# Kernel optimization log

Hardware: AMD Instinct MI355X
Metric: run time of the kernel (lower is better)

Reference implementation:

```python
import jax, jax.numpy as jnp
import numpy as np

D0, D1, D2, D3 = 128, 256, 512, 256
B, L = 64, 1024


def _glorot(key, shape):
    fan_in = shape[0]
    return jax.random.normal(key, shape, dtype=jnp.float32) / np.sqrt(fan_in)


def setup_inputs() -> dict:
    key = jax.random.key(0)
    ks = jax.random.split(key, 16)
    return {
        "hid_r": jax.random.normal(ks[0], (B, L, D3), dtype=jnp.float32),
        "in_mask": jnp.ones((B, L), dtype=jnp.float32),
        "init_in": jnp.zeros((B, 1, D0), dtype=jnp.float32),
        "h0": jnp.zeros((1, B, D2), dtype=jnp.float32),
        "c0": jnp.zeros((1, B, D2), dtype=jnp.float32),
        # lin_1: D0 -> D1 (Linear + ReLU)
        "W1": _glorot(ks[1], (D0, D1)), "b1": jnp.zeros((D1,), jnp.float32),
        # LSTM: input D1, hidden D2, gates order i,f,g,o (PyTorch)
        "Wih": _glorot(ks[2], (D1, 4 * D2)), "Whh": _glorot(ks[3], (D2, 4 * D2)),
        "bih": jnp.zeros((4 * D2,), jnp.float32), "bhh": jnp.zeros((4 * D2,), jnp.float32),
        # lin_2: D2 -> D3
        "W2": _glorot(ks[4], (D2, D3)), "b2": jnp.zeros((D3,), jnp.float32),
        # attention projections q,k,v (D3 -> D3)
        "Wq": _glorot(ks[5], (D3, D3)), "bq": jnp.zeros((D3,), jnp.float32),
        "Wk": _glorot(ks[6], (D3, D3)), "bk": jnp.zeros((D3,), jnp.float32),
        "Wv": _glorot(ks[7], (D3, D3)), "bv": jnp.zeros((D3,), jnp.float32),
        # lin_3: D3 -> D0
        "W3": _glorot(ks[8], (D3, D0)), "b3": jnp.zeros((D0,), jnp.float32),
    }


def reference(hid_r, in_mask, init_in, h0, c0, W1, b1, Wih, Whh, bih, bhh,
              W2, b2, Wq, bq, Wk, bk, Wv, bv, W3, b3):
    length = hid_r.shape[1]
    scale = 1.0 / np.sqrt(D3).astype(np.float32)
    # k/v projections of the (fixed) encoder memory, hoisted out of the loop
    k = hid_r @ Wk + bk            # [B, L, D3]
    v = hid_r @ Wv + bv            # [B, L, D3]
    mask_bias = jnp.where(in_mask == 0, -1e9, 0.0)  # [B, L]

    def step(carry, _):
        h, c, x = carry            # h,c: [B,D2], x: [B,D0]
        a = jax.nn.relu(x @ W1 + b1)                       # lin_1
        gates = a @ Wih + bih + h @ Whh + bhh              # [B, 4*D2]
        i_g, f_g, g_g, o_g = jnp.split(gates, 4, axis=-1)
        c = jax.nn.sigmoid(f_g) * c + jax.nn.sigmoid(i_g) * jnp.tanh(g_g)
        h = jax.nn.sigmoid(o_g) * jnp.tanh(c)
        dx = jax.nn.relu(h @ W2 + b2)                      # lin_2 -> [B,D3]
        q = dx @ Wq + bq                                   # [B, D3]
        scores = jnp.einsum('bd,bld->bl', q, k) * scale + mask_bias
        attn = jax.nn.softmax(scores, axis=-1)             # [B, L]
        ctx = jnp.einsum('bl,bld->bd', attn, v)            # [B, D3]
        y = jax.nn.relu(ctx @ W3 + b3)                     # lin_3 -> [B,D0]
        return (h, c, y), (y, attn)

    carry0 = (h0[0], c0[0], init_in[:, 0, :])
    _, (ys, attns) = jax.lax.scan(step, carry0, None, length=length)
    outputs = jnp.transpose(ys, (1, 0, 2)) * in_mask[:, :, None]  # mask_it
    attention_weights = jnp.transpose(attns, (1, 0, 2))           # [B, L, L]
    return outputs, attention_weights
```

## Files before the change

kernel.cpp:

```cpp
#include <hip/hip_runtime.h>

typedef unsigned short u16;
typedef __attribute__((ext_vector_type(8))) short bf16x8;
typedef __attribute__((ext_vector_type(8))) unsigned short u16x8;
typedef __attribute__((ext_vector_type(4))) unsigned short u16x4;
typedef __attribute__((ext_vector_type(4))) float f32x4;

#define DI static __device__ __forceinline__

constexpr size_t OFF_WKQ  = 0;
constexpr size_t OFF_WVW  = OFF_WKQ  + 256*256*4;
constexpr size_t OFF_WB   = OFF_WVW  + 256*128*4;
constexpr size_t OFF_BYV  = OFF_WB   + 256*4;
constexpr size_t OFF_BG   = OFF_BYV  + 128*4;
constexpr size_t OFF_W2B  = OFF_BG   + 2048*4;
constexpr size_t OFF_W1F  = OFF_W2B  + 512*256*2;
constexpr size_t OFF_WIHF = OFF_W1F  + 16*4*64*8*2;
constexpr size_t OFF_WHHF = OFF_WIHF + 128*8*64*8*2;
constexpr size_t OFF_KT   = OFF_WHHF + 128*16*64*8*2;
constexpr size_t OFF_VW   = OFF_KT   + (size_t)64*1024*256*2;
constexpr size_t OFF_S0   = OFF_VW   + (size_t)64*1024*128*2;
constexpr size_t OFF_CB   = OFF_S0   + 65536*4;
constexpr size_t OFF_HF   = OFF_CB   + 64*512*4;
constexpr size_t OFF_HFR  = OFF_HF   + 64*512*4;
constexpr size_t OFF_SC   = OFF_HFR  + 2*16*4*64*8*2;
constexpr size_t OFF_PART = OFF_SC   + 64*1024*4;

DI float bf2f(u16 u){ unsigned int v = ((unsigned int)u) << 16; return __uint_as_float(v); }
DI u16 f2bf(float f){ unsigned int u = __float_as_uint(f); unsigned int r = (u + 0x7FFFu + ((u>>16)&1u)) >> 16; return (u16)r; }
DI float sigm(float x){ return 1.f/(1.f + __expf(-x)); }
DI float tanh_(float x){ return 1.f - 2.f/(__expf(2.f*x) + 1.f); }

DI int fragIdx(int m, int k){ return (((k>>5)*4 + (m>>4))*64 + ((m&15) | (((k>>3)&3)<<4)))*8 + (k&7); }

__global__ __launch_bounds__(256) void kPrep(char* ws,
    const float* W1, const float* Wih, const float* Whh, const float* W2,
    const float* Wq, const float* bq, const float* Wk, const float* bk,
    const float* Wv, const float* bv, const float* W3, const float* b3,
    const float* bih, const float* bhh, const float* c0, const float* h0)
{
  const int wg = blockIdx.x, tid = threadIdx.x;
  if (wg < 64) {
    float* Wkq = (float*)(ws + OFF_WKQ);
    for (int rr = 0; rr < 4; ++rr) {
      const int e = wg*4 + rr;
      float acc = 0.f;
      for (int d = 0; d < 256; ++d) acc = fmaf(Wk[e*256+d], Wq[tid*256+d], acc);
      Wkq[e*256 + tid] = acc * 0.0625f;
    }
  } else if (wg < 96) {
    float* Wvw = (float*)(ws + OFF_WVW);
    if (tid < 128) {
      for (int rr = 0; rr < 8; ++rr) {
        const int e = (wg-64)*8 + rr;
        float acc = 0.f;
        for (int d = 0; d < 256; ++d) acc = fmaf(Wv[e*256+d], W3[d*128+tid], acc);
        Wvw[e*128 + tid] = acc;
      }
    }
  } else if (wg == 96) {
    float* wb = (float*)(ws + OFF_WB);
    float acc = 0.f;
    for (int d = 0; d < 256; ++d) acc = fmaf(Wk[tid*256+d], bq[d], acc);
    wb[tid] = acc * 0.0625f;
    if (tid < 128) {
      float* byv = (float*)(ws + OFF_BYV);
      float a2 = b3[tid];
      for (int d = 0; d < 256; ++d) a2 = fmaf(bv[d], W3[d*128+tid], a2);
      byv[tid] = a2;
    }
  } else if (wg == 97) {
    float* bg = (float*)(ws + OFF_BG);
    for (int j = tid; j < 2048; j += 256) bg[j] = bih[j] + bhh[j];
  } else if (wg < 106) {
    u16* W2b = (u16*)(ws + OFF_W2B);
    const int r0 = (wg - 98)*64;
    for (int rr = 0; rr < 64; ++rr) W2b[(r0+rr)*256 + tid] = f2bf(W2[(r0+rr)*256 + tid]);
  } else if (wg < 122) {
    u16* W1f = (u16*)(ws + OFF_W1F);
    const int nt2 = wg - 106;
    for (int idx = tid; idx < 4*512; idx += 256) {
      const int kt2 = idx >> 9, rem = idx & 511, lane = rem >> 3, i = rem & 7;
      const int k = kt2*32 + (lane>>4)*8 + i, n = nt2*16 + (lane&15);
      W1f[((nt2*4+kt2)*64+lane)*8+i] = f2bf(W1[k*256+n]);
    }
  } else if (wg < 250) {
    u16* Wihf = (u16*)(ws + OFF_WIHF);
    const int nt = wg - 122;
    for (int idx = tid; idx < 8*512; idx += 256) {
      const int kt = idx >> 9, rem = idx & 511, lane = rem >> 3, i = rem & 7;
      const int k = kt*32 + (lane>>4)*8 + i, r = lane & 15;
      const int gcol = (r>>2)*512 + nt*4 + (r&3);
      Wihf[((nt*8+kt)*64+lane)*8+i] = f2bf(Wih[k*2048 + gcol]);
    }
  } else if (wg < 378) {
    u16* Whhf = (u16*)(ws + OFF_WHHF);
    const int nt = wg - 250;
    for (int idx = tid; idx < 16*512; idx += 256) {
      const int kt = idx >> 9, rem = idx & 511, lane = rem >> 3, i = rem & 7;
      const int k = kt*32 + (lane>>4)*8 + i, r = lane & 15;
      const int gcol = (r>>2)*512 + nt*4 + (r&3);
      Whhf[((nt*16+kt)*64+lane)*8+i] = f2bf(Whh[k*2048 + gcol]);
    }
  } else if (wg < 410) {
    float* cb = (float*)(ws + OFF_CB);
    u16* hfr0 = (u16*)(ws + OFF_HFR);
    const int base = (wg - 378)*1024;
    for (int ii = tid; ii < 1024; ii += 256) {
      const int idx = base + ii, b = idx >> 9, j = idx & 511;
      cb[idx] = c0[idx];
      hfr0[fragIdx(b, j)] = f2bf(h0[idx]);
    }
  }
}

__global__ __launch_bounds__(256) void kKTVW(char* __restrict__ ws, const float* __restrict__ hid_r)
{
  const int wg = blockIdx.x, tid = threadIdx.x;
  __shared__ float lh[256*36];
  const float* Wkq = (const float*)(ws + OFF_WKQ);
  const float* Wvw = (const float*)(ws + OFF_WVW);
  const float* wb  = (const float*)(ws + OFF_WB);
  u16* kt = (u16*)(ws + OFF_KT);
  u16* vw = (u16*)(ws + OFF_VW);
  float* s0 = (float*)(ws + OFF_S0);
  const size_t r0 = (size_t)wg * 32;
  for (int idx = tid; idx < 32*256; idx += 256) {
    const int e = idx & 255, r = idx >> 8;
    lh[e*36 + r] = hid_r[(r0 + r)*256 + e];
  }
  __syncthreads();
  float acc[32];
  #pragma unroll
  for (int r = 0; r < 32; ++r) acc[r] = 0.f;
  for (int e = 0; e < 256; ++e) {
    const float wv = Wkq[e*256 + tid];
    #pragma unroll
    for (int r4 = 0; r4 < 8; ++r4) {
      const float4 l4 = *(const float4*)&lh[e*36 + r4*4];
      acc[r4*4+0] = fmaf(l4.x, wv, acc[r4*4+0]);
      acc[r4*4+1] = fmaf(l4.y, wv, acc[r4*4+1]);
      acc[r4*4+2] = fmaf(l4.z, wv, acc[r4*4+2]);
      acc[r4*4+3] = fmaf(l4.w, wv, acc[r4*4+3]);
    }
  }
  for (int r = 0; r < 32; ++r) kt[(r0 + r)*256 + tid] = f2bf(acc[r]);
  if (tid < 128) {
    #pragma unroll
    for (int r = 0; r < 32; ++r) acc[r] = 0.f;
    for (int e = 0; e < 256; ++e) {
      const float wv = Wvw[e*128 + tid];
      #pragma unroll
      for (int r4 = 0; r4 < 8; ++r4) {
        const float4 l4 = *(const float4*)&lh[e*36 + r4*4];
        acc[r4*4+0] = fmaf(l4.x, wv, acc[r4*4+0]);
        acc[r4*4+1] = fmaf(l4.y, wv, acc[r4*4+1]);
        acc[r4*4+2] = fmaf(l4.z, wv, acc[r4*4+2]);
        acc[r4*4+3] = fmaf(l4.w, wv, acc[r4*4+3]);
      }
    }
    for (int r = 0; r < 32; ++r) vw[(r0 + r)*128 + tid] = f2bf(acc[r]);
  } else if (tid < 160) {
    const int r = tid - 128;
    float a3 = 0.f;
    for (int e = 0; e < 256; ++e) a3 = fmaf(lh[e*36 + r], wb[e], a3);
    s0[r0 + r] = a3;
  }
}

__global__ __launch_bounds__(512) void kA(char* __restrict__ ws, const float* __restrict__ init_in,
    const float* __restrict__ in_mask, const float* __restrict__ b1, float* __restrict__ dout, int s)
{
  const int wg = blockIdx.x, tid = threadIdx.x;
  float* part = (float*)(ws + OFF_PART);
  float* scores = (float*)(ws + OFF_SC);

  if (wg >= 128) {
    if (s == 0) return;
    const int b = (wg - 128) >> 1, half = (wg - 128) & 1;
    float pm[4], pS[4], m = -1e30f;
    #pragma unroll
    for (int c = 0; c < 4; ++c) { pm[c] = part[(b*4+c)*130]; pS[c] = part[(b*4+c)*130+1]; m = fmaxf(m, pm[c]); }
    float Sv = 0.f;
    #pragma unroll
    for (int c = 0; c < 4; ++c) Sv += pS[c] * __expf(pm[c]-m);
    const float inv = 1.f / Sv;
    const int t = s - 1;
    const int l = half*512 + tid;
    float* attn = dout + (size_t)64*1024*128;
    attn[((size_t)b*1024 + t)*1024 + l] = __expf(scores[b*1024 + l] - m) * inv;
    if (half == 0 && tid < 128) {
      const float* byv = (const float*)(ws + OFF_BYV);
      float a2 = 0.f;
      #pragma unroll
      for (int c = 0; c < 4; ++c) a2 += __expf(pm[c]-m) * part[(b*4+c)*130+2+tid];
      const float y = fmaxf(a2*inv + byv[tid], 0.f);
      dout[((size_t)b*1024 + t)*128 + tid] = y * in_mask[b*1024 + t];
    }
    return;
  }

  __shared__ u16 yfrag[4*4*64*8];
  __shared__ u16 afrag[8*4*64*8];
  __shared__ float lfac[64*4];
  __shared__ float gmerge[4*64*4];
  __shared__ float gtile[64*16];
  const float* byv = (const float*)(ws + OFF_BYV);

  if (s == 0) {
    for (int idx = tid; idx < 64*128; idx += 512) {
      const int b = idx >> 7, d0 = idx & 127;
      yfrag[fragIdx(b, d0)] = f2bf(init_in[b*128 + d0]);
    }
  } else {
    if (tid < 64) {
      const int b = tid;
      float pm[4], m = -1e30f;
      #pragma unroll
      for (int c = 0; c < 4; ++c) { pm[c] = part[(b*4+c)*130]; m = fmaxf(m, pm[c]); }
      float Sv = 0.f, pf[4];
      #pragma unroll
      for (int c = 0; c < 4; ++c) { pf[c] = __expf(pm[c]-m); Sv += part[(b*4+c)*130+1]*pf[c]; }
      const float inv = 1.f/Sv;
      #pragma unroll
      for (int c = 0; c < 4; ++c) lfac[b*4+c] = pf[c]*inv;
    }
    __syncthreads();
    for (int idx = tid; idx < 64*128; idx += 512) {
      const int b = idx >> 7, d0 = idx & 127;
      float a2 = byv[d0];
      #pragma unroll
      for (int c = 0; c < 4; ++c) a2 += lfac[b*4+c]*part[(b*4+c)*130+2+d0];
      yfrag[fragIdx(b, d0)] = f2bf(fmaxf(a2, 0.f));
    }
  }
  __syncthreads();

  const int w = tid >> 6, lane = tid & 63;
  {
    const u16* W1f = (const u16*)(ws + OFF_W1F);
    const int mt = w & 3;
    for (int nb = 0; nb < 8; ++nb) {
      const int nt2 = (w>>2)*8 + nb;
      f32x4 acc = {0.f,0.f,0.f,0.f};
      #pragma unroll
      for (int kt2 = 0; kt2 < 4; ++kt2) {
        bf16x8 av = *(const bf16x8*)&yfrag[((kt2*4+mt)*64+lane)*8];
        bf16x8 bv = *(const bf16x8*)&W1f[((nt2*4+kt2)*64+lane)*8];
        acc = __builtin_amdgcn_mfma_f32_16x16x32_bf16(av, bv, acc, 0, 0, 0);
      }
      const int col = nt2*16 + (lane&15);
      const float bb = b1[col];
      #pragma unroll
      for (int i = 0; i < 4; ++i) {
        const int b = mt*16 + (lane>>4)*4 + i;
        afrag[fragIdx(b, col)] = f2bf(fmaxf(acc[i] + bb, 0.f));
      }
    }
  }
  __syncthreads();
  {
    const u16* Wihf = (const u16*)(ws + OFF_WIHF);
    const u16* Whhf = (const u16*)(ws + OFF_WHHF);
    const u16* hfr = (const u16*)(ws + OFF_HFR) + (size_t)(s & 1)*(16*4*64*8);
    const int nt = wg, mt = w & 3;
    f32x4 acc = {0.f,0.f,0.f,0.f};
    if (w < 4) {
      for (int kt = 0; kt < 8; ++kt) {
        bf16x8 av = *(const bf16x8*)&afrag[((kt*4+mt)*64+lane)*8];
        bf16x8 bv = *(const bf16x8*)&Wihf[((nt*8+kt)*64+lane)*8];
        acc = __builtin_amdgcn_mfma_f32_16x16x32_bf16(av, bv, acc, 0, 0, 0);
      }
      for (int kt = 0; kt < 4; ++kt) {
        bf16x8 av = *(const bf16x8*)&hfr[((kt*4+mt)*64+lane)*8];
        bf16x8 bv = *(const bf16x8*)&Whhf[((nt*16+kt)*64+lane)*8];
        acc = __builtin_amdgcn_mfma_f32_16x16x32_bf16(av, bv, acc, 0, 0, 0);
      }
    } else {
      for (int kt = 4; kt < 16; ++kt) {
        bf16x8 av = *(const bf16x8*)&hfr[((kt*4+mt)*64+lane)*8];
        bf16x8 bv = *(const bf16x8*)&Whhf[((nt*16+kt)*64+lane)*8];
        acc = __builtin_amdgcn_mfma_f32_16x16x32_bf16(av, bv, acc, 0, 0, 0);
      }
      #pragma unroll
      for (int i = 0; i < 4; ++i) gmerge[(mt*64+lane)*4+i] = acc[i];
    }
    __syncthreads();
    if (w < 4) {
      const float* bg = (const float*)(ws + OFF_BG);
      const int r = lane & 15;
      const float bb = bg[(r>>2)*512 + nt*4 + (r&3)];
      #pragma unroll
      for (int i = 0; i < 4; ++i) {
        const int b = mt*16 + (lane>>4)*4 + i;
        gtile[b*16 + r] = acc[i] + gmerge[(mt*64+lane)*4+i] + bb;
      }
    }
  }
  __syncthreads();
  if (tid < 256) {
    const int b = tid >> 2, jj = tid & 3;
    const int j = wg*4 + jj;
    const float ig = gtile[b*16 + jj],     fg = gtile[b*16 + 4 + jj];
    const float gg = gtile[b*16 + 8 + jj], og = gtile[b*16 + 12 + jj];
    float* cb = (float*)(ws + OFF_CB);
    float* hf = (float*)(ws + OFF_HF);
    u16* hfw = (u16*)(ws + OFF_HFR) + (size_t)((s & 1) ^ 1)*(16*4*64*8);
    const float cold = cb[b*512 + j];
    const float cnew = sigm(fg)*cold + sigm(ig)*tanh_(gg);
    const float hnew = sigm(og)*tanh_(cnew);
    cb[b*512 + j] = cnew;
    hf[b*512 + j] = hnew;
    hfw[fragIdx(b, j)] = f2bf(hnew);
  }
}

__global__ __launch_bounds__(1024) void kB(char* __restrict__ ws, const float* __restrict__ in_mask,
                                           const float* __restrict__ b2, int s)
{
  const int wg = blockIdx.x, tid = threadIdx.x;
  const int b = wg >> 2, ch = wg & 3;
  __shared__ float red[4*256];
  __shared__ float dxl[256];
  __shared__ float mrg[32*132];
  const float* hf = (const float*)(ws + OFF_HF);
  const u16* W2b = (const u16*)(ws + OFF_W2B);
  (void)s;
  {
    const int n = tid & 255, q = tid >> 8;
    const float* hb = hf + b*512;
    float acc = 0.f;
    #pragma unroll 4
    for (int k = q*128; k < q*128 + 128; ++k)
      acc = fmaf(hb[k], bf2f(W2b[k*256 + n]), acc);
    red[q*256 + n] = acc;
  }
  __syncthreads();
  if (tid < 256) dxl[tid] = fmaxf(red[tid] + red[256+tid] + red[512+tid] + red[768+tid] + b2[tid], 0.f);
  __syncthreads();

  const int hl = tid & 31;
  const int unit = tid >> 5;
  float dxv[8];
  #pragma unroll
  for (int j2 = 0; j2 < 8; ++j2) dxv[j2] = dxl[hl*8 + j2];
  const u16* kt = (const u16*)(ws + OFF_KT);
  const u16* vw = (const u16*)(ws + OFF_VW);
  const float* s0 = (const float*)(ws + OFF_S0);
  float m = -1e30f, S = 0.f, cx0 = 0.f, cx1 = 0.f, cx2 = 0.f, cx3 = 0.f, keep = 0.f;
  for (int i = 0; i < 8; ++i) {
    const int l = ch*256 + i*32 + unit;
    const size_t row = (size_t)b*1024 + l;
    const u16x8 kv = *(const u16x8*)(kt + row*256 + hl*8);
    float sum = 0.f;
    #pragma unroll
    for (int j2 = 0; j2 < 8; ++j2) sum = fmaf(bf2f(kv[j2]), dxv[j2], sum);
    #pragma unroll
    for (int d = 1; d < 32; d <<= 1) sum += __shfl_xor(sum, d, 64);
    float sc = sum + s0[row];
    sc += (in_mask[row] == 0.f) ? -1e9f : 0.f;
    if (hl == i) keep = sc;
    const float mn = fmaxf(m, sc);
    const float cf = __expf(m - mn);
    const float e  = __expf(sc - mn);
    S = S*cf + e;
    cx0 *= cf; cx1 *= cf; cx2 *= cf; cx3 *= cf;
    m = mn;
    const u16x4 vv = *(const u16x4*)(vw + row*128 + hl*4);
    cx0 = fmaf(e, bf2f(vv[0]), cx0);
    cx1 = fmaf(e, bf2f(vv[1]), cx1);
    cx2 = fmaf(e, bf2f(vv[2]), cx2);
    cx3 = fmaf(e, bf2f(vv[3]), cx3);
  }
  if (hl < 8) ((float*)(ws + OFF_SC))[b*1024 + ch*256 + hl*32 + unit] = keep;
  mrg[unit*132 + 4 + hl*4 + 0] = cx0;
  mrg[unit*132 + 4 + hl*4 + 1] = cx1;
  mrg[unit*132 + 4 + hl*4 + 2] = cx2;
  mrg[unit*132 + 4 + hl*4 + 3] = cx3;
  if (hl == 0) { mrg[unit*132] = m; mrg[unit*132+1] = S; }
  __syncthreads();
  if (tid < 128) {
    float mg = -1e30f;
    for (int u = 0; u < 32; ++u) mg = fmaxf(mg, mrg[u*132]);
    float Sg = 0.f, cx = 0.f;
    for (int u = 0; u < 32; ++u) {
      const float f = __expf(mrg[u*132] - mg);
      Sg = fmaf(mrg[u*132+1], f, Sg);
      cx = fmaf(f, mrg[u*132 + 4 + tid], cx);
    }
    float* part = (float*)(ws + OFF_PART);
    part[(b*4+ch)*130 + 2 + tid] = cx;
    if (tid == 0) { part[(b*4+ch)*130] = mg; part[(b*4+ch)*130+1] = Sg; }
  }
}

extern "C" void kernel_launch(void* const* d_in, const int* in_sizes, int n_in,
                              void* d_out, int out_size, void* d_ws, size_t ws_size,
                              hipStream_t stream)
{
  (void)in_sizes; (void)n_in; (void)out_size; (void)ws_size;
  const float* hid_r  = (const float*)d_in[0];
  const float* in_mask= (const float*)d_in[1];
  const float* init_in= (const float*)d_in[2];
  const float* h0     = (const float*)d_in[3];
  const float* c0     = (const float*)d_in[4];
  const float* W1     = (const float*)d_in[5];
  const float* b1     = (const float*)d_in[6];
  const float* Wih    = (const float*)d_in[7];
  const float* Whh    = (const float*)d_in[8];
  const float* bih    = (const float*)d_in[9];
  const float* bhh    = (const float*)d_in[10];
  const float* W2     = (const float*)d_in[11];
  const float* b2     = (const float*)d_in[12];
  const float* Wq     = (const float*)d_in[13];
  const float* bq     = (const float*)d_in[14];
  const float* Wk     = (const float*)d_in[15];
  const float* bk     = (const float*)d_in[16];
  const float* Wv     = (const float*)d_in[17];
  const float* bv     = (const float*)d_in[18];
  const float* W3     = (const float*)d_in[19];
  const float* b3     = (const float*)d_in[20];
  char* ws = (char*)d_ws;
  float* out = (float*)d_out;

  hipLaunchKernelGGL(kPrep, dim3(410), dim3(256), 0, stream, ws,
                     W1, Wih, Whh, W2, Wq, bq, Wk, bk, Wv, bv, W3, b3, bih, bhh, c0, h0);
  hipLaunchKernelGGL(kKTVW, dim3(2048), dim3(256), 0, stream, ws, hid_r);
  for (int s = 0; s < 1024; ++s) {
    hipLaunchKernelGGL(kA, dim3(256), dim3(512), 0, stream, ws, init_in, in_mask, b1, out, s);
    hipLaunchKernelGGL(kB, dim3(256), dim3(1024), 0, stream, ws, in_mask, b2, s);
  }
  hipLaunchKernelGGL(kA, dim3(256), dim3(512), 0, stream, ws, init_in, in_mask, b1, out, 1024);
}
```

Measured before the change: 32.48 ms.

## Fuse the recurrent loop into one persistent per-batch kernel with fp16 dot products

```diff
diff --git a/kernel.cpp b/kernel.cpp
--- a/kernel.cpp
+++ b/kernel.cpp
@@ -1,43 +1,44 @@
 #include <hip/hip_runtime.h>
 
 typedef unsigned short u16;
-typedef __attribute__((ext_vector_type(8))) short bf16x8;
-typedef __attribute__((ext_vector_type(8))) unsigned short u16x8;
-typedef __attribute__((ext_vector_type(4))) unsigned short u16x4;
-typedef __attribute__((ext_vector_type(4))) float f32x4;
+typedef unsigned int u32;
+typedef __attribute__((ext_vector_type(4))) unsigned int u32x4;
+typedef _Float16 half_t;
+typedef __attribute__((ext_vector_type(2))) _Float16 h2;
 
 #define DI static __device__ __forceinline__
 
-constexpr size_t OFF_WKQ  = 0;
-constexpr size_t OFF_WVW  = OFF_WKQ  + 256*256*4;
-constexpr size_t OFF_WB   = OFF_WVW  + 256*128*4;
-constexpr size_t OFF_BYV  = OFF_WB   + 256*4;
-constexpr size_t OFF_BG   = OFF_BYV  + 128*4;
-constexpr size_t OFF_W2B  = OFF_BG   + 2048*4;
-constexpr size_t OFF_W1F  = OFF_W2B  + 512*256*2;
-constexpr size_t OFF_WIHF = OFF_W1F  + 16*4*64*8*2;
-constexpr size_t OFF_WHHF = OFF_WIHF + 128*8*64*8*2;
-constexpr size_t OFF_KT   = OFF_WHHF + 128*16*64*8*2;
-constexpr size_t OFF_VW   = OFF_KT   + (size_t)64*1024*256*2;
-constexpr size_t OFF_S0   = OFF_VW   + (size_t)64*1024*128*2;
-constexpr size_t OFF_CB   = OFF_S0   + 65536*4;
-constexpr size_t OFF_HF   = OFF_CB   + 64*512*4;
-constexpr size_t OFF_HFR  = OFF_HF   + 64*512*4;
-constexpr size_t OFF_SC   = OFF_HFR  + 2*16*4*64*8*2;
-constexpr size_t OFF_PART = OFF_SC   + 64*1024*4;
-
-DI float bf2f(u16 u){ unsigned int v = ((unsigned int)u) << 16; return __uint_as_float(v); }
-DI u16 f2bf(float f){ unsigned int u = __float_as_uint(f); unsigned int r = (u + 0x7FFFu + ((u>>16)&1u)) >> 16; return (u16)r; }
+constexpr size_t OFF_WKQ = 0;
+constexpr size_t OFF_WVW = OFF_WKQ + 256*256*4;
+constexpr size_t OFF_WB  = OFF_WVW + 256*128*4;
+constexpr size_t OFF_BYV = OFF_WB  + 256*4;
+constexpr size_t OFF_BG  = OFF_BYV + 128*4;
+constexpr size_t OFF_W1H = OFF_BG  + 2048*4;
+constexpr size_t OFF_WGH = OFF_W1H + 128*256*2;
+constexpr size_t OFF_W2H = OFF_WGH + 768*2048*2;
+constexpr size_t OFF_S0  = OFF_W2H + 256*512*2;
+constexpr size_t OFF_KT2 = OFF_S0  + 65536*4;
+constexpr size_t OFF_VW2 = OFF_KT2 + (size_t)64*1024*256*2;
+
 DI float sigm(float x){ return 1.f/(1.f + __expf(-x)); }
 DI float tanh_(float x){ return 1.f - 2.f/(__expf(2.f*x) + 1.f); }
-
-DI int fragIdx(int m, int k){ return (((k>>5)*4 + (m>>4))*64 + ((m&15) | (((k>>3)&3)<<4)))*8 + (k&7); }
+DI u16 f2h(float f){ half_t h = (half_t)f; return __builtin_bit_cast(u16, h); }
+DI u32 pk2(float a, float b){ return (u32)f2h(a) | ((u32)f2h(b) << 16); }
+DI h2 u32h2(u32 v){ return __builtin_bit_cast(h2, v); }
+
+DI float fdot2f(h2 a, h2 b, float c){
+#if defined(__has_builtin) && __has_builtin(__builtin_amdgcn_fdot2)
+  return __builtin_amdgcn_fdot2(a, b, c, false);
+#else
+  return c + (float)a[0]*(float)b[0] + (float)a[1]*(float)b[1];
+#endif
+}
 
 __global__ __launch_bounds__(256) void kPrep(char* ws,
     const float* W1, const float* Wih, const float* Whh, const float* W2,
     const float* Wq, const float* bq, const float* Wk, const float* bk,
     const float* Wv, const float* bv, const float* W3, const float* b3,
-    const float* bih, const float* bhh, const float* c0, const float* h0)
+    const float* bih, const float* bhh)
 {
   const int wg = blockIdx.x, tid = threadIdx.x;
   if (wg < 64) {
@@ -73,56 +74,42 @@
     float* bg = (float*)(ws + OFF_BG);
     for (int j = tid; j < 2048; j += 256) bg[j] = bih[j] + bhh[j];
   } else if (wg < 106) {
-    u16* W2b = (u16*)(ws + OFF_W2B);
-    const int r0 = (wg - 98)*64;
-    for (int rr = 0; rr < 64; ++rr) W2b[(r0+rr)*256 + tid] = f2bf(W2[(r0+rr)*256 + tid]);
-  } else if (wg < 122) {
-    u16* W1f = (u16*)(ws + OFF_W1F);
-    const int nt2 = wg - 106;
-    for (int idx = tid; idx < 4*512; idx += 256) {
-      const int kt2 = idx >> 9, rem = idx & 511, lane = rem >> 3, i = rem & 7;
-      const int k = kt2*32 + (lane>>4)*8 + i, n = nt2*16 + (lane&15);
-      W1f[((nt2*4+kt2)*64+lane)*8+i] = f2bf(W1[k*256+n]);
-    }
-  } else if (wg < 250) {
-    u16* Wihf = (u16*)(ws + OFF_WIHF);
-    const int nt = wg - 122;
-    for (int idx = tid; idx < 8*512; idx += 256) {
-      const int kt = idx >> 9, rem = idx & 511, lane = rem >> 3, i = rem & 7;
-      const int k = kt*32 + (lane>>4)*8 + i, r = lane & 15;
-      const int gcol = (r>>2)*512 + nt*4 + (r&3);
-      Wihf[((nt*8+kt)*64+lane)*8+i] = f2bf(Wih[k*2048 + gcol]);
-    }
-  } else if (wg < 378) {
-    u16* Whhf = (u16*)(ws + OFF_WHHF);
-    const int nt = wg - 250;
-    for (int idx = tid; idx < 16*512; idx += 256) {
-      const int kt = idx >> 9, rem = idx & 511, lane = rem >> 3, i = rem & 7;
-      const int k = kt*32 + (lane>>4)*8 + i, r = lane & 15;
-      const int gcol = (r>>2)*512 + nt*4 + (r&3);
-      Whhf[((nt*16+kt)*64+lane)*8+i] = f2bf(Whh[k*2048 + gcol]);
-    }
-  } else if (wg < 410) {
-    float* cb = (float*)(ws + OFF_CB);
-    u16* hfr0 = (u16*)(ws + OFF_HFR);
-    const int base = (wg - 378)*1024;
-    for (int ii = tid; ii < 1024; ii += 256) {
-      const int idx = base + ii, b = idx >> 9, j = idx & 511;
-      cb[idx] = c0[idx];
-      hfr0[fragIdx(b, j)] = f2bf(h0[idx]);
-    }
-  }
-}
-
-__global__ __launch_bounds__(256) void kKTVW(char* __restrict__ ws, const float* __restrict__ hid_r)
+    u16* W1h = (u16*)(ws + OFF_W1H);
+    const int k0 = (wg - 98)*16;
+    for (int kk = 0; kk < 16; ++kk) {
+      const int k = k0 + kk;
+      W1h[((k>>3)*256 + tid)*8 + (k&7)] = f2h(W1[k*256 + tid]);
+    }
+  } else if (wg < 170) {
+    u16* Wgh = (u16*)(ws + OFF_WGH);
+    const int k0 = (wg - 106)*12;
+    for (int kk = 0; kk < 12; ++kk) {
+      const int k = k0 + kk;
+      for (int n = tid; n < 2048; n += 256) {
+        const float src = (k < 256) ? Wih[k*2048 + n] : Whh[(k-256)*2048 + n];
+        Wgh[((k>>3)*2048 + n)*8 + (k&7)] = f2h(src);
+      }
+    }
+  } else if (wg < 178) {
+    u16* W2h = (u16*)(ws + OFF_W2H);
+    const int n0 = (wg - 170)*32;
+    for (int nn = 0; nn < 32; ++nn) {
+      const int n = n0 + nn;
+      for (int k = tid; k < 512; k += 256) W2h[n*512 + k] = f2h(W2[k*256 + n]);
+    }
+  }
+}
+
+__global__ __launch_bounds__(256) void kKTVW(char* __restrict__ ws, const float* __restrict__ hid_r,
+                                             const float* __restrict__ in_mask)
 {
   const int wg = blockIdx.x, tid = threadIdx.x;
   __shared__ float lh[256*36];
   const float* Wkq = (const float*)(ws + OFF_WKQ);
   const float* Wvw = (const float*)(ws + OFF_WVW);
   const float* wb  = (const float*)(ws + OFF_WB);
-  u16* kt = (u16*)(ws + OFF_KT);
-  u16* vw = (u16*)(ws + OFF_VW);
+  u16* kt2 = (u16*)(ws + OFF_KT2);
+  u16* vw2 = (u16*)(ws + OFF_VW2);
   float* s0 = (float*)(ws + OFF_S0);
   const size_t r0 = (size_t)wg * 32;
   for (int idx = tid; idx < 32*256; idx += 256) {
@@ -144,7 +131,12 @@
       acc[r4*4+3] = fmaf(l4.w, wv, acc[r4*4+3]);
     }
   }
-  for (int r = 0; r < 32; ++r) kt[(r0 + r)*256 + tid] = f2bf(acc[r]);
+  for (int r = 0; r < 32; ++r) {
+    const size_t row = r0 + r;
+    const size_t bb = row >> 10;
+    const int l = (int)(row & 1023);
+    kt2[(((bb*32) + (size_t)(tid>>3))*1024 + l)*8 + (tid&7)] = f2h(acc[r]);
+  }
   if (tid < 128) {
     #pragma unroll
     for (int r = 0; r < 32; ++r) acc[r] = 0.f;
@@ -159,238 +151,206 @@
         acc[r4*4+3] = fmaf(l4.w, wv, acc[r4*4+3]);
       }
     }
-    for (int r = 0; r < 32; ++r) vw[(r0 + r)*128 + tid] = f2bf(acc[r]);
+    for (int r = 0; r < 32; ++r) {
+      const size_t row = r0 + r;
+      const size_t bb = row >> 10;
+      const int l = (int)(row & 1023);
+      vw2[((bb*512) + (size_t)(l>>1))*256 + tid*2 + (l&1)] = f2h(acc[r]);
+    }
   } else if (tid < 160) {
     const int r = tid - 128;
     float a3 = 0.f;
     for (int e = 0; e < 256; ++e) a3 = fmaf(lh[e*36 + r], wb[e], a3);
-    s0[r0 + r] = a3;
-  }
-}
-
-__global__ __launch_bounds__(512) void kA(char* __restrict__ ws, const float* __restrict__ init_in,
-    const float* __restrict__ in_mask, const float* __restrict__ b1, float* __restrict__ dout, int s)
+    s0[r0 + r] = a3 + (in_mask[r0 + r] == 0.f ? -1e9f : 0.f);
+  }
+}
+
+__global__ __launch_bounds__(1024) void kMain(char* __restrict__ ws, const float* __restrict__ init_in,
+    const float* __restrict__ in_mask, const float* __restrict__ b1g, const float* __restrict__ b2g,
+    const float* __restrict__ h0, const float* __restrict__ c0, float* __restrict__ dout)
 {
-  const int wg = blockIdx.x, tid = threadIdx.x;
-  float* part = (float*)(ws + OFF_PART);
-  float* scores = (float*)(ws + OFF_SC);
-
-  if (wg >= 128) {
-    if (s == 0) return;
-    const int b = (wg - 128) >> 1, half = (wg - 128) & 1;
-    float pm[4], pS[4], m = -1e30f;
-    #pragma unroll
-    for (int c = 0; c < 4; ++c) { pm[c] = part[(b*4+c)*130]; pS[c] = part[(b*4+c)*130+1]; m = fmaxf(m, pm[c]); }
-    float Sv = 0.f;
-    #pragma unroll
-    for (int c = 0; c < 4; ++c) Sv += pS[c] * __expf(pm[c]-m);
-    const float inv = 1.f / Sv;
-    const int t = s - 1;
-    const int l = half*512 + tid;
-    float* attn = dout + (size_t)64*1024*128;
-    attn[((size_t)b*1024 + t)*1024 + l] = __expf(scores[b*1024 + l] - m) * inv;
-    if (half == 0 && tid < 128) {
-      const float* byv = (const float*)(ws + OFF_BYV);
-      float a2 = 0.f;
-      #pragma unroll
-      for (int c = 0; c < 4; ++c) a2 += __expf(pm[c]-m) * part[(b*4+c)*130+2+tid];
-      const float y = fmaxf(a2*inv + byv[tid], 0.f);
-      dout[((size_t)b*1024 + t)*128 + tid] = y * in_mask[b*1024 + t];
-    }
-    return;
-  }
-
-  __shared__ u16 yfrag[4*4*64*8];
-  __shared__ u16 afrag[8*4*64*8];
-  __shared__ float lfac[64*4];
-  __shared__ float gmerge[4*64*4];
-  __shared__ float gtile[64*16];
+  const int b = blockIdx.x, tid = threadIdx.x;
+  const int hl = tid & 31, unit = tid >> 5;
+
+  __shared__ __align__(16) u32 x2[384];
+  __shared__ __align__(16) u32 yh2[64];
+  __shared__ __align__(16) u32 dxh2[128];
+  __shared__ __align__(16) u32 eh2[512];
+  __shared__ float gt[2048];
+  __shared__ float cst[512];
+  __shared__ float s0l[1024];
+  __shared__ float sc[1024];
+  __shared__ float red[256*33];
+  __shared__ float mrg[32*132];
+  __shared__ float rtmp[64];
+  __shared__ float fin[2];
+
+  const u16* W1h = (const u16*)(ws + OFF_W1H);
+  const u16* Wgh = (const u16*)(ws + OFF_WGH);
+  const u16* W2h = (const u16*)(ws + OFF_W2H);
+  const u16* kt2 = (const u16*)(ws + OFF_KT2) + (size_t)b*32*1024*8;
+  const u16* vw2 = (const u16*)(ws + OFF_VW2) + (size_t)b*512*256;
+  const float* s0g = (const float*)(ws + OFF_S0) + b*1024;
+  const float* bgg = (const float*)(ws + OFF_BG);
   const float* byv = (const float*)(ws + OFF_BYV);
-
-  if (s == 0) {
-    for (int idx = tid; idx < 64*128; idx += 512) {
-      const int b = idx >> 7, d0 = idx & 127;
-      yfrag[fragIdx(b, d0)] = f2bf(init_in[b*128 + d0]);
-    }
-  } else {
+  float* attn = dout + (size_t)64*1024*128;
+
+  if (tid < 512) cst[tid] = c0[b*512 + tid];
+  if (tid < 256) x2[128 + tid] = pk2(h0[b*512 + 2*tid], h0[b*512 + 2*tid + 1]);
+  if (tid < 64)  yh2[tid] = pk2(init_in[b*128 + 2*tid], init_in[b*128 + 2*tid + 1]);
+  s0l[tid] = s0g[tid];
+  __syncthreads();
+
+  for (int s = 0; s < 1024; ++s) {
+    if (tid < 256) {
+      float acc = b1g[tid];
+      #pragma unroll 4
+      for (int r = 0; r < 16; ++r) {
+        const u32x4 wv = *(const u32x4*)(W1h + ((r*256 + tid) << 3));
+        const u32x4 xq = *(const u32x4*)&yh2[r*4];
+        acc = fdot2f(u32h2(wv[0]), u32h2(xq[0]), acc);
+        acc = fdot2f(u32h2(wv[1]), u32h2(xq[1]), acc);
+        acc = fdot2f(u32h2(wv[2]), u32h2(xq[2]), acc);
+        acc = fdot2f(u32h2(wv[3]), u32h2(xq[3]), acc);
+      }
+      ((u16*)x2)[tid] = f2h(fmaxf(acc, 0.f));
+    }
+    __syncthreads();
+    {
+      float g0 = bgg[tid], g1 = bgg[tid + 1024];
+      #pragma unroll 4
+      for (int r = 0; r < 96; ++r) {
+        const u32x4 w0 = *(const u32x4*)(Wgh + (((r << 11) + tid) << 3));
+        const u32x4 w1 = *(const u32x4*)(Wgh + (((r << 11) + tid + 1024) << 3));
+        const u32x4 xq = *(const u32x4*)&x2[r*4];
+        g0 = fdot2f(u32h2(w0[0]), u32h2(xq[0]), g0);
+        g0 = fdot2f(u32h2(w0[1]), u32h2(xq[1]), g0);
+        g0 = fdot2f(u32h2(w0[2]), u32h2(xq[2]), g0);
+        g0 = fdot2f(u32h2(w0[3]), u32h2(xq[3]), g0);
+        g1 = fdot2f(u32h2(w1[0]), u32h2(xq[0]), g1);
+        g1 = fdot2f(u32h2(w1[1]), u32h2(xq[1]), g1);
+        g1 = fdot2f(u32h2(w1[2]), u32h2(xq[2]), g1);
+        g1 = fdot2f(u32h2(w1[3]), u32h2(xq[3]), g1);
+      }
+      gt[tid] = g0; gt[tid + 1024] = g1;
+    }
+    __syncthreads();
+    if (tid < 512) {
+      const float gi = gt[tid], gf = gt[512 + tid], gg = gt[1024 + tid], go = gt[1536 + tid];
+      const float cn = sigm(gf)*cst[tid] + sigm(gi)*tanh_(gg);
+      const float h  = sigm(go)*tanh_(cn);
+      cst[tid] = cn;
+      ((u16*)x2)[256 + tid] = f2h(h);
+    }
+    __syncthreads();
+    {
+      const u32x4 ha = *(const u32x4*)&x2[128 + hl*8];
+      const u32x4 hb = *(const u32x4*)&x2[128 + hl*8 + 4];
+      #pragma unroll
+      for (int j = 0; j < 8; ++j) {
+        const int n = unit*8 + j;
+        const u32x4 w0 = *(const u32x4*)(W2h + n*512 + hl*16);
+        const u32x4 w1 = *(const u32x4*)(W2h + n*512 + hl*16 + 8);
+        float acc = 0.f;
+        acc = fdot2f(u32h2(ha[0]), u32h2(w0[0]), acc);
+        acc = fdot2f(u32h2(ha[1]), u32h2(w0[1]), acc);
+        acc = fdot2f(u32h2(ha[2]), u32h2(w0[2]), acc);
+        acc = fdot2f(u32h2(ha[3]), u32h2(w0[3]), acc);
+        acc = fdot2f(u32h2(hb[0]), u32h2(w1[0]), acc);
+        acc = fdot2f(u32h2(hb[1]), u32h2(w1[1]), acc);
+        acc = fdot2f(u32h2(hb[2]), u32h2(w1[2]), acc);
+        acc = fdot2f(u32h2(hb[3]), u32h2(w1[3]), acc);
+        red[n*33 + hl] = acc;
+      }
+    }
+    __syncthreads();
+    if (tid < 256) {
+      float a = 0.f;
+      #pragma unroll
+      for (int l = 0; l < 32; ++l) a += red[tid*33 + l];
+      const float dx = fmaxf(a + b2g[tid], 0.f);
+      ((u16*)dxh2)[tid] = f2h(dx);
+    }
+    __syncthreads();
+    {
+      float st = s0l[tid];
+      #pragma unroll 4
+      for (int r = 0; r < 32; ++r) {
+        const u32x4 kv = __builtin_nontemporal_load((const u32x4*)(kt2 + (((size_t)r << 10) + tid)*8));
+        const u32x4 xq = *(const u32x4*)&dxh2[r*4];
+        st = fdot2f(u32h2(kv[0]), u32h2(xq[0]), st);
+        st = fdot2f(u32h2(kv[1]), u32h2(xq[1]), st);
+        st = fdot2f(u32h2(kv[2]), u32h2(xq[2]), st);
+        st = fdot2f(u32h2(kv[3]), u32h2(xq[3]), st);
+      }
+      sc[tid] = st;
+    }
+    __syncthreads();
     if (tid < 64) {
-      const int b = tid;
-      float pm[4], m = -1e30f;
-      #pragma unroll
-      for (int c = 0; c < 4; ++c) { pm[c] = part[(b*4+c)*130]; m = fmaxf(m, pm[c]); }
-      float Sv = 0.f, pf[4];
-      #pragma unroll
-      for (int c = 0; c < 4; ++c) { pf[c] = __expf(pm[c]-m); Sv += part[(b*4+c)*130+1]*pf[c]; }
-      const float inv = 1.f/Sv;
-      #pragma unroll
-      for (int c = 0; c < 4; ++c) lfac[b*4+c] = pf[c]*inv;
-    }
-    __syncthreads();
-    for (int idx = tid; idx < 64*128; idx += 512) {
-      const int b = idx >> 7, d0 = idx & 127;
-      float a2 = byv[d0];
-      #pragma unroll
-      for (int c = 0; c < 4; ++c) a2 += lfac[b*4+c]*part[(b*4+c)*130+2+d0];
-      yfrag[fragIdx(b, d0)] = f2bf(fmaxf(a2, 0.f));
-    }
-  }
-  __syncthreads();
-
-  const int w = tid >> 6, lane = tid & 63;
-  {
-    const u16* W1f = (const u16*)(ws + OFF_W1F);
-    const int mt = w & 3;
-    for (int nb = 0; nb < 8; ++nb) {
-      const int nt2 = (w>>2)*8 + nb;
-      f32x4 acc = {0.f,0.f,0.f,0.f};
-      #pragma unroll
-      for (int kt2 = 0; kt2 < 4; ++kt2) {
-        bf16x8 av = *(const bf16x8*)&yfrag[((kt2*4+mt)*64+lane)*8];
-        bf16x8 bv = *(const bf16x8*)&W1f[((nt2*4+kt2)*64+lane)*8];
-        acc = __builtin_amdgcn_mfma_f32_16x16x32_bf16(av, bv, acc, 0, 0, 0);
-      }
-      const int col = nt2*16 + (lane&15);
-      const float bb = b1[col];
-      #pragma unroll
-      for (int i = 0; i < 4; ++i) {
-        const int b = mt*16 + (lane>>4)*4 + i;
-        afrag[fragIdx(b, col)] = f2bf(fmaxf(acc[i] + bb, 0.f));
-      }
-    }
-  }
-  __syncthreads();
-  {
-    const u16* Wihf = (const u16*)(ws + OFF_WIHF);
-    const u16* Whhf = (const u16*)(ws + OFF_WHHF);
-    const u16* hfr = (const u16*)(ws + OFF_HFR) + (size_t)(s & 1)*(16*4*64*8);
-    const int nt = wg, mt = w & 3;
-    f32x4 acc = {0.f,0.f,0.f,0.f};
-    if (w < 4) {
-      for (int kt = 0; kt < 8; ++kt) {
-        bf16x8 av = *(const bf16x8*)&afrag[((kt*4+mt)*64+lane)*8];
-        bf16x8 bv = *(const bf16x8*)&Wihf[((nt*8+kt)*64+lane)*8];
-        acc = __builtin_amdgcn_mfma_f32_16x16x32_bf16(av, bv, acc, 0, 0, 0);
-      }
-      for (int kt = 0; kt < 4; ++kt) {
-        bf16x8 av = *(const bf16x8*)&hfr[((kt*4+mt)*64+lane)*8];
-        bf16x8 bv = *(const bf16x8*)&Whhf[((nt*16+kt)*64+lane)*8];
-        acc = __builtin_amdgcn_mfma_f32_16x16x32_bf16(av, bv, acc, 0, 0, 0);
-      }
-    } else {
-      for (int kt = 4; kt < 16; ++kt) {
-        bf16x8 av = *(const bf16x8*)&hfr[((kt*4+mt)*64+lane)*8];
-        bf16x8 bv = *(const bf16x8*)&Whhf[((nt*16+kt)*64+lane)*8];
-        acc = __builtin_amdgcn_mfma_f32_16x16x32_bf16(av, bv, acc, 0, 0, 0);
-      }
-      #pragma unroll
-      for (int i = 0; i < 4; ++i) gmerge[(mt*64+lane)*4+i] = acc[i];
-    }
-    __syncthreads();
-    if (w < 4) {
-      const float* bg = (const float*)(ws + OFF_BG);
-      const int r = lane & 15;
-      const float bb = bg[(r>>2)*512 + nt*4 + (r&3)];
-      #pragma unroll
-      for (int i = 0; i < 4; ++i) {
-        const int b = mt*16 + (lane>>4)*4 + i;
-        gtile[b*16 + r] = acc[i] + gmerge[(mt*64+lane)*4+i] + bb;
-      }
-    }
-  }
-  __syncthreads();
-  if (tid < 256) {
-    const int b = tid >> 2, jj = tid & 3;
-    const int j = wg*4 + jj;
-    const float ig = gtile[b*16 + jj],     fg = gtile[b*16 + 4 + jj];
-    const float gg = gtile[b*16 + 8 + jj], og = gtile[b*16 + 12 + jj];
-    float* cb = (float*)(ws + OFF_CB);
-    float* hf = (float*)(ws + OFF_HF);
-    u16* hfw = (u16*)(ws + OFF_HFR) + (size_t)((s & 1) ^ 1)*(16*4*64*8);
-    const float cold = cb[b*512 + j];
-    const float cnew = sigm(fg)*cold + sigm(ig)*tanh_(gg);
-    const float hnew = sigm(og)*tanh_(cnew);
-    cb[b*512 + j] = cnew;
-    hf[b*512 + j] = hnew;
-    hfw[fragIdx(b, j)] = f2bf(hnew);
-  }
-}
-
-__global__ __launch_bounds__(1024) void kB(char* __restrict__ ws, const float* __restrict__ in_mask,
-                                           const float* __restrict__ b2, int s)
-{
-  const int wg = blockIdx.x, tid = threadIdx.x;
-  const int b = wg >> 2, ch = wg & 3;
-  __shared__ float red[4*256];
-  __shared__ float dxl[256];
-  __shared__ float mrg[32*132];
-  const float* hf = (const float*)(ws + OFF_HF);
-  const u16* W2b = (const u16*)(ws + OFF_W2B);
-  (void)s;
-  {
-    const int n = tid & 255, q = tid >> 8;
-    const float* hb = hf + b*512;
-    float acc = 0.f;
-    #pragma unroll 4
-    for (int k = q*128; k < q*128 + 128; ++k)
-      acc = fmaf(hb[k], bf2f(W2b[k*256 + n]), acc);
-    red[q*256 + n] = acc;
-  }
-  __syncthreads();
-  if (tid < 256) dxl[tid] = fmaxf(red[tid] + red[256+tid] + red[512+tid] + red[768+tid] + b2[tid], 0.f);
-  __syncthreads();
-
-  const int hl = tid & 31;
-  const int unit = tid >> 5;
-  float dxv[8];
-  #pragma unroll
-  for (int j2 = 0; j2 < 8; ++j2) dxv[j2] = dxl[hl*8 + j2];
-  const u16* kt = (const u16*)(ws + OFF_KT);
-  const u16* vw = (const u16*)(ws + OFF_VW);
-  const float* s0 = (const float*)(ws + OFF_S0);
-  float m = -1e30f, S = 0.f, cx0 = 0.f, cx1 = 0.f, cx2 = 0.f, cx3 = 0.f, keep = 0.f;
-  for (int i = 0; i < 8; ++i) {
-    const int l = ch*256 + i*32 + unit;
-    const size_t row = (size_t)b*1024 + l;
-    const u16x8 kv = *(const u16x8*)(kt + row*256 + hl*8);
-    float sum = 0.f;
-    #pragma unroll
-    for (int j2 = 0; j2 < 8; ++j2) sum = fmaf(bf2f(kv[j2]), dxv[j2], sum);
-    #pragma unroll
-    for (int d = 1; d < 32; d <<= 1) sum += __shfl_xor(sum, d, 64);
-    float sc = sum + s0[row];
-    sc += (in_mask[row] == 0.f) ? -1e9f : 0.f;
-    if (hl == i) keep = sc;
-    const float mn = fmaxf(m, sc);
-    const float cf = __expf(m - mn);
-    const float e  = __expf(sc - mn);
-    S = S*cf + e;
-    cx0 *= cf; cx1 *= cf; cx2 *= cf; cx3 *= cf;
-    m = mn;
-    const u16x4 vv = *(const u16x4*)(vw + row*128 + hl*4);
-    cx0 = fmaf(e, bf2f(vv[0]), cx0);
-    cx1 = fmaf(e, bf2f(vv[1]), cx1);
-    cx2 = fmaf(e, bf2f(vv[2]), cx2);
-    cx3 = fmaf(e, bf2f(vv[3]), cx3);
-  }
-  if (hl < 8) ((float*)(ws + OFF_SC))[b*1024 + ch*256 + hl*32 + unit] = keep;
-  mrg[unit*132 + 4 + hl*4 + 0] = cx0;
-  mrg[unit*132 + 4 + hl*4 + 1] = cx1;
-  mrg[unit*132 + 4 + hl*4 + 2] = cx2;
-  mrg[unit*132 + 4 + hl*4 + 3] = cx3;
-  if (hl == 0) { mrg[unit*132] = m; mrg[unit*132+1] = S; }
-  __syncthreads();
-  if (tid < 128) {
-    float mg = -1e30f;
-    for (int u = 0; u < 32; ++u) mg = fmaxf(mg, mrg[u*132]);
-    float Sg = 0.f, cx = 0.f;
-    for (int u = 0; u < 32; ++u) {
-      const float f = __expf(mrg[u*132] - mg);
-      Sg = fmaf(mrg[u*132+1], f, Sg);
-      cx = fmaf(f, mrg[u*132 + 4 + tid], cx);
-    }
-    float* part = (float*)(ws + OFF_PART);
-    part[(b*4+ch)*130 + 2 + tid] = cx;
-    if (tid == 0) { part[(b*4+ch)*130] = mg; part[(b*4+ch)*130+1] = Sg; }
+      float m = -1e30f;
+      #pragma unroll
+      for (int i = 0; i < 16; ++i) m = fmaxf(m, sc[tid*16 + i]);
+      rtmp[tid] = m;
+    }
+    __syncthreads();
+    if (tid < 64) {
+      float m = rtmp[tid];
+      #pragma unroll
+      for (int d = 32; d >= 1; d >>= 1) m = fmaxf(m, __shfl_xor(m, d, 64));
+      if (tid == 0) fin[0] = m;
+    }
+    __syncthreads();
+    {
+      const float e = __expf(sc[tid] - fin[0]);
+      sc[tid] = e;
+      ((u16*)eh2)[tid] = f2h(e);
+    }
+    __syncthreads();
+    if (tid < 64) {
+      float ssum = 0.f;
+      #pragma unroll
+      for (int i = 0; i < 16; ++i) ssum += sc[tid*16 + i];
+      rtmp[tid] = ssum;
+    }
+    __syncthreads();
+    if (tid < 64) {
+      float ssum = rtmp[tid];
+      #pragma unroll
+      for (int d = 32; d >= 1; d >>= 1) ssum += __shfl_xor(ssum, d, 64);
+      if (tid == 0) fin[1] = ssum;
+    }
+    __syncthreads();
+    {
+      float cx0 = 0.f, cx1 = 0.f, cx2 = 0.f, cx3 = 0.f;
+      #pragma unroll 4
+      for (int lp = 0; lp < 16; ++lp) {
+        const int lpi = unit*16 + lp;
+        const u32x4 vv = __builtin_nontemporal_load((const u32x4*)(vw2 + lpi*256 + hl*8));
+        const h2 e2 = u32h2(eh2[lpi]);
+        cx0 = fdot2f(e2, u32h2(vv[0]), cx0);
+        cx1 = fdot2f(e2, u32h2(vv[1]), cx1);
+        cx2 = fdot2f(e2, u32h2(vv[2]), cx2);
+        cx3 = fdot2f(e2, u32h2(vv[3]), cx3);
+      }
+      mrg[unit*132 + 4 + hl*4 + 0] = cx0;
+      mrg[unit*132 + 4 + hl*4 + 1] = cx1;
+      mrg[unit*132 + 4 + hl*4 + 2] = cx2;
+      mrg[unit*132 + 4 + hl*4 + 3] = cx3;
+    }
+    __syncthreads();
+    {
+      const float inv = 1.f / fin[1];
+      __builtin_nontemporal_store(sc[tid]*inv, &attn[((size_t)b*1024 + s)*1024 + tid]);
+      if (tid < 128) {
+        float cxs = 0.f;
+        #pragma unroll
+        for (int u = 0; u < 32; ++u) cxs += mrg[u*132 + 4 + tid];
+        const float y = fmaxf(cxs*inv + byv[tid], 0.f);
+        __builtin_nontemporal_store(y*in_mask[b*1024 + s], &dout[((size_t)b*1024 + s)*128 + tid]);
+        ((u16*)yh2)[tid] = f2h(y);
+      }
+    }
+    __syncthreads();
   }
 }
 
@@ -423,12 +383,9 @@
   char* ws = (char*)d_ws;
   float* out = (float*)d_out;
 
-  hipLaunchKernelGGL(kPrep, dim3(410), dim3(256), 0, stream, ws,
-                     W1, Wih, Whh, W2, Wq, bq, Wk, bk, Wv, bv, W3, b3, bih, bhh, c0, h0);
-  hipLaunchKernelGGL(kKTVW, dim3(2048), dim3(256), 0, stream, ws, hid_r);
-  for (int s = 0; s < 1024; ++s) {
-    hipLaunchKernelGGL(kA, dim3(256), dim3(512), 0, stream, ws, init_in, in_mask, b1, out, s);
-    hipLaunchKernelGGL(kB, dim3(256), dim3(1024), 0, stream, ws, in_mask, b2, s);
-  }
-  hipLaunchKernelGGL(kA, dim3(256), dim3(512), 0, stream, ws, init_in, in_mask, b1, out, 1024);
-}
+  hipLaunchKernelGGL(kPrep, dim3(178), dim3(256), 0, stream, ws,
+                     W1, Wih, Whh, W2, Wq, bq, Wk, bk, Wv, bv, W3, b3, bih, bhh);
+  hipLaunchKernelGGL(kKTVW, dim3(2048), dim3(256), 0, stream, ws, hid_r, in_mask);
+  hipLaunchKernelGGL(kMain, dim3(64), dim3(1024), 0, stream, ws,
+                     init_in, in_mask, b1, b2, h0, c0, out);
+}
```

Result: slower. 55.41 ms (+70.6%).
